# Optimization experiments

Hardware: AMD Instinct MI355X
Metric: run time of the kernel (lower is better)

Reference implementation:

```python
import jax, jax.numpy as jnp
import numpy as np

H_DIM = 64
NUM_ROTATIONS = 128


def setup_inputs() -> dict:
    key = jax.random.key(0)
    k1, k2 = jax.random.split(key)
    x = jax.random.normal(k1, (8, 4096, 16, H_DIM), dtype=jnp.float32)
    thetas = jax.random.normal(k2, (NUM_ROTATIONS,), dtype=jnp.float32)
    return {"x": x, "thetas": thetas}


def reference(x, thetas):
    # x: [B, S, nH, h_dim]. Original does x @ G_k for k in range(num_rotations),
    # where G_k is identity except rows/cols (i, j) = (k % h, (k+1) % h):
    #   (xG)[:, i] =  cos*x_i + sin*x_j
    #   (xG)[:, j] = -sin*x_i + cos*x_j
    # Rotations are sequential (consecutive k share a column), so use lax.scan
    # and touch only the two affected columns instead of a full GEMM.
    B, S, nH, D = x.shape
    K = thetas.shape[0]
    xf = x.reshape(-1, D)  # [N, h_dim]
    ks = jnp.arange(K, dtype=jnp.int32)
    idx_i = ks % D
    idx_j = (ks + 1) % D

    def step(xc, inp):
        i, j, th = inp
        c, s = jnp.cos(th), jnp.sin(th)
        xi = xc[:, i]
        xj = xc[:, j]
        xc = xc.at[:, i].set(c * xi + s * xj).at[:, j].set(-s * xi + c * xj)
        return xc, None

    xf, _ = jax.lax.scan(step, xf, (idx_i, idx_j, thetas))
    return xf.reshape(B, S, nH, D)
```

## Files before the change

kernel.cpp:

```cpp
#include <hip/hip_runtime.h>

#define D_DIM 64
#define N_ROT 128

typedef float v4f __attribute__((ext_vector_type(4)));

__global__ __launch_bounds__(64) void givens_kernel(
    const float* __restrict__ x,
    const float* __restrict__ thetas,
    float* __restrict__ out,
    int nchunks)
{
    __shared__ __align__(16) float bufA[64 * D_DIM];
    __shared__ __align__(16) float bufB[64 * D_DIM];
    __shared__ float2 cs_tab[N_ROT];

    const int l    = threadIdx.x;
    const int lo16 = l & 15;

    {
        const float tha = thetas[l];
        const float thb = thetas[l + 64];
        cs_tab[l]      = make_float2(cosf(tha), sinf(tha));
        cs_tab[l + 64] = make_float2(cosf(thb), sinf(thb));
    }
    asm volatile("s_waitcnt lgkmcnt(0)" ::: "memory");

    const int cpb = (nchunks + gridDim.x - 1) / gridDim.x;
    const int c0  = blockIdx.x * cpb;
    const int c1  = (c0 + cpb < nchunks) ? (c0 + cpb) : nchunks;
    if (c0 >= c1) return;

    auto STAGE = [&](int c) {
        const char* g = (const char*)(x + (size_t)c * (64 * D_DIM));
        #pragma unroll
        for (int q = 0; q < 16; ++q) {
            const int r  = q * 4 + (l >> 4);
            const int gs = lo16 ^ (r & 15);
            __builtin_amdgcn_global_load_lds(
                (const __attribute__((address_space(1))) void*)(g + r * 256 + gs * 16),
                (__attribute__((address_space(3))) void*)((char*)bufA + q * 1024),
                16, 0, 0);
        }
    };

    float v[D_DIM];

    auto GATHER = [&]() {
        #pragma unroll
        for (int g = 0; g < 16; ++g) {
            const int sl = g ^ lo16;
            const float4 t = *reinterpret_cast<const float4*>(&bufA[l * D_DIM + sl * 4]);
            v[4 * g + 0] = t.x; v[4 * g + 1] = t.y;
            v[4 * g + 2] = t.z; v[4 * g + 3] = t.w;
        }
    };

    STAGE(c0);
    asm volatile("s_waitcnt vmcnt(0)" ::: "memory");
    GATHER();
    asm volatile("s_waitcnt lgkmcnt(0)" ::: "memory");
    if (c0 + 1 < c1) STAGE(c0 + 1);

    for (int c = c0; c < c1; ++c) {
        #pragma unroll
        for (int k = 0; k < N_ROT; ++k) {
            const int i = k & (D_DIM - 1);
            const int j = (k + 1) & (D_DIM - 1);
            const float2 cs = cs_tab[k];
            const float xi = v[i], xj = v[j];
            v[i] = fmaf(cs.x, xi, cs.y * xj);
            v[j] = fmaf(-cs.y, xi, cs.x * xj);
        }

        #pragma unroll
        for (int g = 0; g < 16; ++g) {
            const int sl = g ^ lo16;
            float4 t;
            t.x = v[4 * g + 0]; t.y = v[4 * g + 1];
            t.z = v[4 * g + 2]; t.w = v[4 * g + 3];
            *reinterpret_cast<float4*>(&bufB[l * D_DIM + sl * 4]) = t;
        }
        asm volatile("s_waitcnt lgkmcnt(0)" ::: "memory");

        {
            char* gout = (char*)(out + (size_t)c * (64 * D_DIM));
            #pragma unroll
            for (int q = 0; q < 16; ++q) {
                const int r  = q * 4 + (l >> 4);
                const int gs = lo16 ^ (r & 15);
                const v4f t = *reinterpret_cast<const v4f*>(&bufB[q * 256 + l * 4]);
                __builtin_nontemporal_store(
                    t, reinterpret_cast<v4f*>(gout + r * 256 + gs * 16));
            }
        }

        if (c + 1 < c1) {
            asm volatile("s_waitcnt vmcnt(16)" ::: "memory");
            GATHER();
            asm volatile("s_waitcnt lgkmcnt(0)" ::: "memory");
            if (c + 2 < c1) STAGE(c + 2);
        }
    }
}

extern "C" void kernel_launch(void* const* d_in, const int* in_sizes, int n_in,
                              void* d_out, int out_size, void* d_ws, size_t ws_size,
                              hipStream_t stream) {
    const float* x      = (const float*)d_in[0];
    const float* thetas = (const float*)d_in[1];
    float* out          = (float*)d_out;

    const int nrows   = in_sizes[0] / D_DIM;
    const int nchunks = nrows / 64;

    int grid = 4 * 256;
    if (grid > nchunks) grid = nchunks;

    givens_kernel<<<grid, 64, 0, stream>>>(x, thetas, out, nchunks);
}
```

Measured before the change: 48.70 us.

## Split each row across two lanes with shuffle-based cross-half rotations

Each row is now handled by a pair of lanes, each holding 32 of the 64 columns in registers, so a block processes 32-row chunks and the grid doubles. Rotations inside one half are applied with a predicated select, and the two rotations that cross the halves use a lane shuffle. This cuts per-thread register pressure and LDS use per block to raise occupancy and memory-level parallelism. In exchange, every rotation is computed by both lanes with one result discarded, and the serial dependency chain gains shuffles.

After: 50.96 us. 4.6% more time.

```diff
diff --git a/kernel.cpp b/kernel.cpp
--- a/kernel.cpp
+++ b/kernel.cpp
@@ -11,12 +11,14 @@
     float* __restrict__ out,
     int nchunks)
 {
-    __shared__ __align__(16) float bufA[64 * D_DIM];
-    __shared__ __align__(16) float bufB[64 * D_DIM];
+    __shared__ __align__(16) float bufA[32 * D_DIM];
+    __shared__ __align__(16) float bufB[32 * D_DIM];
     __shared__ float2 cs_tab[N_ROT];
 
-    const int l    = threadIdx.x;
-    const int lo16 = l & 15;
+    const int l  = threadIdx.x;
+    const int r  = l >> 1;
+    const int h  = l & 1;
+    const int r7 = r & 7;
 
     {
         const float tha = thetas[l];
@@ -32,25 +34,26 @@
     if (c0 >= c1) return;
 
     auto STAGE = [&](int c) {
-        const char* g = (const char*)(x + (size_t)c * (64 * D_DIM));
+        const char* g = (const char*)(x + (size_t)c * (32 * D_DIM));
         #pragma unroll
-        for (int q = 0; q < 16; ++q) {
-            const int r  = q * 4 + (l >> 4);
-            const int gs = lo16 ^ (r & 15);
+        for (int q = 0; q < 8; ++q) {
+            const int row = q * 4 + (l >> 4);
+            const int p   = l & 15;
+            const int vs  = (p & 8) | ((p & 7) ^ (row & 7));
             __builtin_amdgcn_global_load_lds(
-                (const __attribute__((address_space(1))) void*)(g + r * 256 + gs * 16),
+                (const __attribute__((address_space(1))) void*)(g + row * 256 + vs * 16),
                 (__attribute__((address_space(3))) void*)((char*)bufA + q * 1024),
                 16, 0, 0);
         }
     };
 
-    float v[D_DIM];
+    float v[32];
 
     auto GATHER = [&]() {
         #pragma unroll
-        for (int g = 0; g < 16; ++g) {
-            const int sl = g ^ lo16;
-            const float4 t = *reinterpret_cast<const float4*>(&bufA[l * D_DIM + sl * 4]);
+        for (int g = 0; g < 8; ++g) {
+            const int ph = (h << 3) | (g ^ r7);
+            const float4 t = *reinterpret_cast<const float4*>(&bufA[r * D_DIM + ph * 4]);
             v[4 * g + 0] = t.x; v[4 * g + 1] = t.y;
             v[4 * g + 2] = t.z; v[4 * g + 3] = t.w;
         }
@@ -66,37 +69,60 @@
         #pragma unroll
         for (int k = 0; k < N_ROT; ++k) {
             const int i = k & (D_DIM - 1);
-            const int j = (k + 1) & (D_DIM - 1);
             const float2 cs = cs_tab[k];
-            const float xi = v[i], xj = v[j];
-            v[i] = fmaf(cs.x, xi, cs.y * xj);
-            v[j] = fmaf(-cs.y, xi, cs.x * xj);
+            const float cc = cs.x, ss = cs.y;
+            if ((i & 31) != 31) {
+                const int  li  = i & 31;
+                const bool act = (h == (i >> 5));
+                const float xi = v[li], xj = v[li + 1];
+                const float ni = fmaf(cc, xi, ss * xj);
+                const float nj = fmaf(-ss, xi, cc * xj);
+                v[li]     = act ? ni : v[li];
+                v[li + 1] = act ? nj : v[li + 1];
+            } else if (i == 31) {
+                const float other = __shfl_xor(h ? v[0] : v[31], 1);
+                const float xi = h ? other : v[31];
+                const float xj = h ? v[0]  : other;
+                const float ni = fmaf(cc, xi, ss * xj);
+                const float nj = fmaf(-ss, xi, cc * xj);
+                v[31] = h ? v[31] : ni;
+                v[0]  = h ? nj    : v[0];
+            } else {
+                const float other = __shfl_xor(h ? v[31] : v[0], 1);
+                const float xi = h ? v[31] : other;
+                const float xj = h ? other : v[0];
+                const float ni = fmaf(cc, xi, ss * xj);
+                const float nj = fmaf(-ss, xi, cc * xj);
+                v[31] = h ? ni   : v[31];
+                v[0]  = h ? v[0] : nj;
+            }
         }
 
         #pragma unroll
-        for (int g = 0; g < 16; ++g) {
-            const int sl = g ^ lo16;
+        for (int g = 0; g < 8; ++g) {
+            const int ph = (h << 3) | (g ^ r7);
             float4 t;
             t.x = v[4 * g + 0]; t.y = v[4 * g + 1];
             t.z = v[4 * g + 2]; t.w = v[4 * g + 3];
-            *reinterpret_cast<float4*>(&bufB[l * D_DIM + sl * 4]) = t;
+            *reinterpret_cast<float4*>(&bufB[r * D_DIM + ph * 4]) = t;
         }
         asm volatile("s_waitcnt lgkmcnt(0)" ::: "memory");
 
         {
-            char* gout = (char*)(out + (size_t)c * (64 * D_DIM));
+            char* gout = (char*)(out + (size_t)c * (32 * D_DIM));
             #pragma unroll
-            for (int q = 0; q < 16; ++q) {
-                const int r  = q * 4 + (l >> 4);
-                const int gs = lo16 ^ (r & 15);
+            for (int q = 0; q < 8; ++q) {
+                const int row = q * 4 + (l >> 4);
+                const int p   = l & 15;
+                const int vs  = (p & 8) | ((p & 7) ^ (row & 7));
                 const v4f t = *reinterpret_cast<const v4f*>(&bufB[q * 256 + l * 4]);
                 __builtin_nontemporal_store(
-                    t, reinterpret_cast<v4f*>(gout + r * 256 + gs * 16));
+                    t, reinterpret_cast<v4f*>(gout + row * 256 + vs * 16));
             }
         }
 
         if (c + 1 < c1) {
-            asm volatile("s_waitcnt vmcnt(16)" ::: "memory");
+            asm volatile("s_waitcnt vmcnt(8)" ::: "memory");
             GATHER();
             asm volatile("s_waitcnt lgkmcnt(0)" ::: "memory");
             if (c + 2 < c1) STAGE(c + 2);
@@ -112,9 +138,9 @@
     float* out          = (float*)d_out;
 
     const int nrows   = in_sizes[0] / D_DIM;
-    const int nchunks = nrows / 64;
+    const int nchunks = nrows / 32;
 
-    int grid = 4 * 256;
+    int grid = 8 * 256;
     if (grid > nchunks) grid = nchunks;
 
     givens_kernel<<<grid, 64, 0, stream>>>(x, thetas, out, nchunks);
```
